# Kernel optimization log

Measured on AMD Instinct MI355X. Metric: run time of the kernel, lower is better.

## Reference

```python
import jax, jax.numpy as jnp
import numpy as np

B, Hh, Ww, C = 16, 56, 56, 256
NH, WS, SS = 8, 7, 3
HD = C // NH
N = WS * WS
SCALE = HD ** -0.5
EPS = 1e-5


def _rel_pos_index():
    coords = np.stack(np.meshgrid(np.arange(WS), np.arange(WS), indexing='ij'))  # (2, ws, ws)
    cf = coords.reshape(2, -1)
    rc = (cf[:, :, None] - cf[:, None, :]).transpose(1, 2, 0).astype(np.int64)  # (N, N, 2)
    rc[:, :, 0] += WS - 1
    rc[:, :, 1] += WS - 1
    rc[:, :, 0] *= 2 * WS - 1
    return jnp.asarray(rc.sum(-1))  # (N, N)

REL_IDX = _rel_pos_index()


def _shift_mask():
    # standard Swin SW-MSA mask for cyclic shift
    img = np.zeros((1, Hh, Ww, 1), dtype=np.float32)
    cnt = 0
    for hs in (slice(0, -WS), slice(-WS, -SS), slice(-SS, None)):
        for ws_ in (slice(0, -WS), slice(-WS, -SS), slice(-SS, None)):
            img[:, hs, ws_, :] = cnt
            cnt += 1
    mw = img.reshape(1, Hh // WS, WS, Ww // WS, WS, 1).transpose(0, 1, 3, 2, 4, 5).reshape(-1, N)
    am = mw[:, None, :] - mw[:, :, None]
    return jnp.asarray(np.where(am != 0, -100.0, 0.0).astype(np.float32))  # (nW, N, N)


def _ln(x, g, b):
    mu = x.mean(-1, keepdims=True)
    var = ((x - mu) ** 2).mean(-1, keepdims=True)
    return (x - mu) * jax.lax.rsqrt(var + EPS) * g + b


def setup_inputs() -> dict:
    key = jax.random.key(0)
    ks = jax.random.split(key, 8)
    return {
        'x': jax.random.normal(ks[0], (B, Hh * Ww, C), jnp.float32),
        'mask': _shift_mask(),
        'norm1_g': jnp.ones((C,), jnp.float32),
        'norm1_b': jnp.zeros((C,), jnp.float32),
        'qkv_w': jax.random.normal(ks[1], (3 * C, C), jnp.float32) * 0.02,
        'qkv_b': jnp.zeros((3 * C,), jnp.float32),
        'rel_bias': jax.random.normal(ks[2], ((2 * WS - 1) ** 2, NH), jnp.float32) * 0.02,
        'proj_w': jax.random.normal(ks[3], (C, C), jnp.float32) * 0.02,
        'proj_b': jnp.zeros((C,), jnp.float32),
        'norm2_g': jnp.ones((C,), jnp.float32),
        'norm2_b': jnp.zeros((C,), jnp.float32),
        'fc1_w': jax.random.normal(ks[4], (4 * C, C), jnp.float32) * 0.02,
        'fc1_b': jnp.zeros((4 * C,), jnp.float32),
        'fc2_w': jax.random.normal(ks[5], (C, 4 * C), jnp.float32) * 0.02,
        'fc2_b': jnp.zeros((C,), jnp.float32),
    }


def reference(x, mask, norm1_g, norm1_b, qkv_w, qkv_b, rel_bias, proj_w, proj_b,
              norm2_g, norm2_b, fc1_w, fc1_b, fc2_w, fc2_b):
    shortcut = x
    h = _ln(x, norm1_g, norm1_b).reshape(B, Hh, Ww, C)
    # cyclic shift
    h = jnp.roll(h, (-SS, -SS), axis=(1, 2))
    # window partition -> (B*nW, N, C)
    hw = h.reshape(B, Hh // WS, WS, Ww // WS, WS, C).transpose(0, 1, 3, 2, 4, 5).reshape(-1, N, C)
    # qkv projection
    qkv = (hw @ qkv_w.T + qkv_b).reshape(-1, N, 3, NH, HD).transpose(2, 0, 3, 1, 4)
    q, k, v = qkv[0] * SCALE, qkv[1], qkv[2]  # (Bw, NH, N, HD)
    attn = jnp.einsum('bhnd,bhmd->bhnm', q, k)  # (Bw, NH, N, N)
    rpb = rel_bias[REL_IDX.reshape(-1)].reshape(N, N, NH).transpose(2, 0, 1)
    attn = attn + rpb[None]
    nW = mask.shape[0]
    attn = attn.reshape(B, nW, NH, N, N) + mask[None, :, None]
    attn = jax.nn.softmax(attn.reshape(-1, NH, N, N), axis=-1)
    o = jnp.einsum('bhnm,bhmd->bhnd', attn, v).transpose(0, 2, 1, 3).reshape(-1, N, C)
    o = o @ proj_w.T + proj_b
    # window reverse
    o = o.reshape(B, Hh // WS, Ww // WS, WS, WS, C).transpose(0, 1, 3, 2, 4, 5).reshape(B, Hh, Ww, C)
    o = jnp.roll(o, (SS, SS), axis=(1, 2)).reshape(B, Hh * Ww, C)
    x = shortcut + o
    h2 = _ln(x, norm2_g, norm2_b)
    h2 = jax.nn.gelu(h2 @ fc1_w.T + fc1_b, approximate=False)
    return x + (h2 @ fc2_w.T + fc2_b)
```

## Files before the change

### kernel.cpp

```cpp
#include <hip/hip_runtime.h>
#include <cmath>

#define B_    16
#define HH    56
#define WWI   56
#define C_    256
#define NH_   8
#define WS_   7
#define SS_   3
#define HD_   32
#define NTOK  50176
#define NN    49
#define SCALE_ 0.17677669529663689f
#define EPS_  1e-5f

typedef __bf16  bf16x8  __attribute__((ext_vector_type(8)));
typedef float   f32x4   __attribute__((ext_vector_type(4)));
typedef unsigned short ushort8v __attribute__((ext_vector_type(8)));

__device__ __forceinline__ unsigned short f2bf(float f) {
    unsigned int u = __float_as_uint(f);
    unsigned int r = u + 0x7FFFu + ((u >> 16) & 1u);
    return (unsigned short)(r >> 16);
}
__device__ __forceinline__ float bf2f(unsigned short h) {
    return __uint_as_float(((unsigned int)h) << 16);
}
__device__ __forceinline__ float gelu_t(float x) {
    float t = 0.7978845608028654f * (x + 0.044715f * x * x * x);
    float e = __expf(2.0f * t);
    float th = 1.0f - 2.0f * __builtin_amdgcn_rcpf(e + 1.0f);
    return 0.5f * x * (1.0f + th);
}

__device__ __forceinline__ void gload_lds16(const unsigned short* g, unsigned short* l) {
    __builtin_amdgcn_global_load_lds(
        (const __attribute__((address_space(1))) unsigned int*)g,
        (__attribute__((address_space(3))) unsigned int*)l, 16, 0, 0);
}

__global__ __launch_bounds__(256) void convw_k(
    const float* __restrict__ qkvw, const float* __restrict__ projw,
    const float* __restrict__ fc1w, const float* __restrict__ fc2w,
    unsigned short* __restrict__ dst)
{
    int i = blockIdx.x * 256 + threadIdx.x;
    float v;
    if      (i < 196608) v = qkvw[i];
    else if (i < 262144) v = projw[i - 196608];
    else if (i < 524288) v = fc1w[i - 262144];
    else                 v = fc2w[i - 524288];
    dst[i] = f2bf(v);
}

__global__ __launch_bounds__(256) void cb_k(
    const float* __restrict__ mask, const float* __restrict__ relb,
    unsigned short* __restrict__ cb)
{
    int s = blockIdx.x;
    int wi = s >> 3, head = s & 7;
    for (int p = threadIdx.x; p < 2408; p += 256) {
        float v = 0.0f;
        if (p < 2401) {
            int i = p / NN, j = p - i * NN;
            int di = i / 7 - j / 7 + 6, dj = i % 7 - j % 7 + 6;
            v = relb[(di * 13 + dj) * NH_ + head] + mask[(size_t)wi * 2401 + p];
        }
        cb[(size_t)s * 2408 + p] = f2bf(v);
    }
}

__global__ __launch_bounds__(256) void ln_k(
    const float* __restrict__ x, const float* __restrict__ g,
    const float* __restrict__ bta, unsigned short* __restrict__ dst, int shifted)
{
    int wave = threadIdx.x >> 6, lane = threadIdx.x & 63;
    int tok = blockIdx.x * 4 + wave;
    const float4 v = *(const float4*)(x + (size_t)tok * C_ + lane * 4);
    float s = v.x + v.y + v.z + v.w;
    float q = v.x*v.x + v.y*v.y + v.z*v.z + v.w*v.w;
    for (int o = 32; o > 0; o >>= 1) { s += __shfl_xor(s, o, 64); q += __shfl_xor(q, o, 64); }
    float mu  = s * (1.0f / C_);
    float var = q * (1.0f / C_) - mu * mu;
    float rs  = rsqrtf(var + EPS_);
    float4 gg = *(const float4*)(g   + lane * 4);
    float4 bb = *(const float4*)(bta + lane * 4);
    float y0 = (v.x - mu) * rs * gg.x + bb.x;
    float y1 = (v.y - mu) * rs * gg.y + bb.y;
    float y2 = (v.z - mu) * rs * gg.z + bb.z;
    float y3 = (v.w - mu) * rs * gg.w + bb.w;
    size_t di;
    if (shifted) {
        int b = tok / 3136, p = tok % 3136;
        int ph = p / 56, pw = p % 56;
        int sh = ph - SS_; if (sh < 0) sh += HH;
        int sw = pw - SS_; if (sw < 0) sw += WWI;
        int bw = b * 64 + (sh / WS_) * 8 + (sw / WS_);
        int n  = (sh % WS_) * WS_ + (sw % WS_);
        di = ((size_t)bw * NN + n) * C_ + lane * 4;
    } else {
        di = (size_t)tok * C_ + lane * 4;
    }
    unsigned int lo = (unsigned int)f2bf(y0) | ((unsigned int)f2bf(y1) << 16);
    unsigned int hi = (unsigned int)f2bf(y2) | ((unsigned int)f2bf(y3) << 16);
    uint2 u; u.x = lo; u.y = hi;
    *(uint2*)(dst + di) = u;
}

template<int EPI, int NT>
__global__ __launch_bounds__(256) void gemm_k(
    const unsigned short* __restrict__ A, const unsigned short* __restrict__ Bt,
    int K, const float* __restrict__ bias,
    const float* __restrict__ resid, float* __restrict__ outF,
    unsigned short* __restrict__ outQ, unsigned short* __restrict__ outK,
    unsigned short* __restrict__ outV)
{
    __shared__ __align__(16) unsigned char smem[49152];
    const int tid = threadIdx.x;
    const int lin = blockIdx.x;
    const int xcd = lin & 7, t = lin >> 3;
    const int m0 = (xcd * 49 + t / NT) * 128;
    const int n0 = (t % NT) * 128;
    const int wave = tid >> 6, lane = tid & 63, quad = lane >> 4, l16 = lane & 15;
    const int wm = wave >> 1, wn = wave & 1;
    const int r0 = tid >> 2, c0 = (tid & 3) * 8;

    const size_t gA0 = (size_t)(m0 + r0) * K + c0;
    const size_t gA1 = (size_t)(m0 + r0 + 64) * K + c0;
    const size_t gB0 = (size_t)(n0 + r0) * K + c0;
    const size_t gB1 = (size_t)(n0 + r0 + 64) * K + c0;
    const int woff = wave * 512;

    f32x4 acc[4][4] = {};
    const int nk = K >> 5;
    #pragma unroll
    for (int p = 0; p < 2; ++p) {
        unsigned short* sA = (unsigned short*)(smem + p * 16384);
        unsigned short* sB = sA + 4096;
        const int kp = p << 5;
        gload_lds16(A + gA0 + kp, sA + woff);
        gload_lds16(A + gA1 + kp, sA + woff + 2048);
        gload_lds16(Bt + gB0 + kp, sB + woff);
        gload_lds16(Bt + gB1 + kp, sB + woff + 2048);
    }
    int bufc = 0;
    for (int kk = 0; kk < nk; ++kk) {
        if (kk + 2 < nk) {
            int bufn = bufc + 2; if (bufn >= 3) bufn -= 3;
            unsigned short* sA = (unsigned short*)(smem + bufn * 16384);
            unsigned short* sB = sA + 4096;
            const int k2 = (kk + 2) << 5;
            gload_lds16(A + gA0 + k2, sA + woff);
            gload_lds16(A + gA1 + k2, sA + woff + 2048);
            gload_lds16(Bt + gB0 + k2, sB + woff);
            gload_lds16(Bt + gB1 + k2, sB + woff + 2048);
            __asm volatile("s_waitcnt vmcnt(8)\n\ts_barrier" ::: "memory");
        } else if (kk + 1 < nk) {
            __asm volatile("s_waitcnt vmcnt(4)\n\ts_barrier" ::: "memory");
        } else {
            __asm volatile("s_waitcnt vmcnt(0)\n\ts_barrier" ::: "memory");
        }
        const unsigned short* sA = (const unsigned short*)(smem + bufc * 16384);
        const unsigned short* sB = sA + 4096;
        bf16x8 af[4], bfr[4];
        #pragma unroll
        for (int tt = 0; tt < 4; ++tt) {
            af[tt]  = __builtin_bit_cast(bf16x8, *(const ushort8v*)(sA + (wm * 64 + tt * 16 + l16) * 32 + quad * 8));
            bfr[tt] = __builtin_bit_cast(bf16x8, *(const ushort8v*)(sB + (wn * 64 + tt * 16 + l16) * 32 + quad * 8));
        }
        #pragma unroll
        for (int mt = 0; mt < 4; ++mt)
            #pragma unroll
            for (int nt = 0; nt < 4; ++nt)
                acc[mt][nt] = __builtin_amdgcn_mfma_f32_16x16x32_bf16(af[mt], bfr[nt], acc[mt][nt], 0, 0, 0);
        __asm volatile("s_barrier" ::: "memory");
        if (++bufc == 3) bufc = 0;
    }

    float b4[4];
    #pragma unroll
    for (int nt = 0; nt < 4; ++nt) b4[nt] = bias[n0 + wn * 64 + nt * 16 + l16];

    if (EPI == 0 || EPI == 2) {
        unsigned short (*swB)[136] = (unsigned short (*)[136])smem;
        const int seg = n0 >> 8;
        const float qs = (EPI == 0 && seg == 0) ? SCALE_ : 1.0f;
        #pragma unroll
        for (int mt = 0; mt < 4; ++mt)
            #pragma unroll
            for (int nt = 0; nt < 4; ++nt)
                #pragma unroll
                for (int r = 0; r < 4; ++r) {
                    float v = acc[mt][nt][r] + b4[nt];
                    if (EPI == 0) v *= qs; else v = gelu_t(v);
                    swB[wm * 64 + mt * 16 + quad * 4 + r][wn * 64 + nt * 16 + l16] = f2bf(v);
                }
        __syncthreads();
        if (EPI == 0) {
            unsigned short* dstp = seg == 0 ? outQ : (seg == 1 ? outK : outV);
            const int nbase = n0 & 255;
            for (int tt = tid; tt < 2048; tt += 256) {
                int row = tt >> 4, c8 = (tt & 15) * 8;
                int m = m0 + row, bw = m / NN, nw = m - bw * NN;
                int cc = nbase + c8;
                uint4 u = *(uint4*)&swB[row][c8];
                *(uint4*)&dstp[(((size_t)bw * NH_ + (cc >> 5)) * NN + nw) * HD_ + (cc & 31)] = u;
            }
        } else {
            for (int tt = tid; tt < 2048; tt += 256) {
                int row = tt >> 4, c8 = (tt & 15) * 8;
                uint4 u = *(uint4*)&swB[row][c8];
                *(uint4*)&outQ[(size_t)(m0 + row) * 1024 + n0 + c8] = u;
            }
        }
    } else {
        float (*swF)[132] = (float (*)[132])smem;
        #pragma unroll
        for (int p = 0; p < 2; ++p) {
            __syncthreads();
            if (wm == p) {
                #pragma unroll
                for (int mt = 0; mt < 4; ++mt)
                    #pragma unroll
                    for (int nt = 0; nt < 4; ++nt)
                        #pragma unroll
                        for (int r = 0; r < 4; ++r)
                            swF[mt * 16 + quad * 4 + r][wn * 64 + nt * 16 + l16] = acc[mt][nt][r] + b4[nt];
            }
            __syncthreads();
            for (int tt = tid; tt < 2048; tt += 256) {
                int rl = tt >> 5, c4 = (tt & 31) * 4;
                size_t adr;
                if (EPI == 1) {
                    int m = m0 + p * 64 + rl, bw = m / NN, nw = m - bw * NN;
                    int b = bw >> 6, wi = bw & 63;
                    int sh = (wi >> 3) * WS_ + nw / WS_;
                    int sw = (wi & 7) * WS_ + nw % WS_;
                    int ph = sh + SS_; if (ph >= HH)  ph -= HH;
                    int pw = sw + SS_; if (pw >= WWI) pw -= WWI;
                    adr = ((size_t)b * 3136 + ph * 56 + pw) * C_ + n0 + c4;
                } else {
                    adr = (size_t)(m0 + p * 64 + rl) * C_ + n0 + c4;
                }
                float4 u = *(float4*)&swF[rl][c4];
                const float4 rr = (EPI == 1) ? *(const float4*)&resid[adr]
                                             : *(const float4*)&outF[adr];
                u.x += rr.x; u.y += rr.y; u.z += rr.z; u.w += rr.w;
                *(float4*)&outF[adr] = u;
            }
        }
    }
}

__global__ __launch_bounds__(256) void attn_k(
    const unsigned short* __restrict__ qb, const unsigned short* __restrict__ kb,
    const unsigned short* __restrict__ vb, const unsigned short* __restrict__ cb,
    unsigned short* __restrict__ ob)
{
    __shared__ unsigned short qs[64][40];
    __shared__ unsigned short ks[64][40];
    __shared__ unsigned short vt[32][72];
    __shared__ unsigned short sp[64][72];
    __shared__ unsigned short cbs[2408];
    const int tid = threadIdx.x;
    const int bw = blockIdx.x >> 3, head = blockIdx.x & 7;
    const size_t base = (size_t)blockIdx.x * (NN * HD_);

    for (int t = tid; t < 588; t += 256) {
        int seg = t / 196, idx = t - seg * 196;
        int e = idx * 8;
        const unsigned short* src = (seg == 0 ? qb : seg == 1 ? kb : vb) + base + e;
        uint4 u = *(const uint4*)src;
        if (seg == 0)      *(uint4*)&qs[e >> 5][e & 31] = u;
        else if (seg == 1) *(uint4*)&ks[e >> 5][e & 31] = u;
        else {
            int n = e >> 5, hd = e & 31;
            const unsigned short* pu = (const unsigned short*)&u;
            #pragma unroll
            for (int uu = 0; uu < 8; ++uu) vt[hd + uu][n] = pu[uu];
        }
    }
    {
        const unsigned short* cbase = cb + (size_t)(((bw & 63) * 8 + head)) * 2408;
        for (int t = tid; t < 301; t += 256)
            *(uint4*)&cbs[t * 8] = *(const uint4*)(cbase + t * 8);
        for (int t = tid; t < 480; t += 256) vt[t / 15][NN + t % 15] = 0;
    }
    __syncthreads();

    const int wave = tid >> 6, lane = tid & 63, quad = lane >> 4, l16 = lane & 15;
    const f32x4 zz = {};

    bf16x8 afq = __builtin_bit_cast(bf16x8, *(const ushort8v*)&qs[wave * 16 + l16][quad * 8]);
    f32x4 s4[4];
    #pragma unroll
    for (int jt = 0; jt < 4; ++jt) {
        bf16x8 bk = __builtin_bit_cast(bf16x8, *(const ushort8v*)&ks[jt * 16 + l16][quad * 8]);
        s4[jt] = __builtin_amdgcn_mfma_f32_16x16x32_bf16(afq, bk, zz, 0, 0, 0);
    }

    #pragma unroll
    for (int r = 0; r < 4; ++r) {
        int i = wave * 16 + quad * 4 + r;
        float vals[4];
        #pragma unroll
        for (int jt = 0; jt < 4; ++jt) {
            int j = jt * 16 + l16;
            vals[jt] = (i < NN && j < NN) ? s4[jt][r] + bf2f(cbs[i * NN + j]) : -1e30f;
        }
        float mx = fmaxf(fmaxf(vals[0], vals[1]), fmaxf(vals[2], vals[3]));
        #pragma unroll
        for (int o = 1; o < 16; o <<= 1) mx = fmaxf(mx, __shfl_xor(mx, o, 64));
        float e[4], sum = 0.0f;
        #pragma unroll
        for (int jt = 0; jt < 4; ++jt) { e[jt] = __expf(vals[jt] - mx); sum += e[jt]; }
        #pragma unroll
        for (int o = 1; o < 16; o <<= 1) sum += __shfl_xor(sum, o, 64);
        float inv = 1.0f / sum;
        #pragma unroll
        for (int jt = 0; jt < 4; ++jt) sp[i][jt * 16 + l16] = f2bf(e[jt] * inv);
    }
    __syncthreads();

    bf16x8 ap[2];
    #pragma unroll
    for (int kt = 0; kt < 2; ++kt)
        ap[kt] = __builtin_bit_cast(bf16x8, *(const ushort8v*)&sp[wave * 16 + l16][kt * 32 + quad * 8]);
    f32x4 o4[2] = {};
    #pragma unroll
    for (int nt = 0; nt < 2; ++nt)
        #pragma unroll
        for (int kt = 0; kt < 2; ++kt) {
            bf16x8 bv = __builtin_bit_cast(bf16x8, *(const ushort8v*)&vt[nt * 16 + l16][kt * 32 + quad * 8]);
            o4[nt] = __builtin_amdgcn_mfma_f32_16x16x32_bf16(ap[kt], bv, o4[nt], 0, 0, 0);
        }
    #pragma unroll
    for (int nt = 0; nt < 2; ++nt)
        #pragma unroll
        for (int r = 0; r < 4; ++r) {
            int i = wave * 16 + quad * 4 + r;
            if (i < NN)
                ob[((size_t)bw * NN + i) * C_ + head * HD_ + nt * 16 + l16] = f2bf(o4[nt][r]);
        }
}

extern "C" void kernel_launch(void* const* d_in, const int* in_sizes, int n_in,
                              void* d_out, int out_size, void* d_ws, size_t ws_size,
                              hipStream_t stream)
{
    const float* x     = (const float*)d_in[0];
    const float* mask  = (const float*)d_in[1];
    const float* n1g   = (const float*)d_in[2];
    const float* n1b   = (const float*)d_in[3];
    const float* qkvw  = (const float*)d_in[4];
    const float* qkvb  = (const float*)d_in[5];
    const float* relb  = (const float*)d_in[6];
    const float* projw = (const float*)d_in[7];
    const float* projb = (const float*)d_in[8];
    const float* n2g   = (const float*)d_in[9];
    const float* n2b   = (const float*)d_in[10];
    const float* fc1w  = (const float*)d_in[11];
    const float* fc1b  = (const float*)d_in[12];
    const float* fc2w  = (const float*)d_in[13];
    const float* fc2b  = (const float*)d_in[14];
    float* out = (float*)d_out;

    unsigned short* wq = (unsigned short*)d_ws;
    unsigned short* wp = wq + 196608;
    unsigned short* w1 = wq + 262144;
    unsigned short* w2 = wq + 524288;
    unsigned short* hw = wq + 786432;
    unsigned short* qb = hw + 12845056;
    unsigned short* kb = qb + 12845056;
    unsigned short* vb = kb + 12845056;
    unsigned short* ob = vb + 12845056;
    unsigned short* h2 = ob + 12845056;
    unsigned short* a1 = h2 + 12845056;
    unsigned short* cbt = a1;

    convw_k<<<3072, 256, 0, stream>>>(qkvw, projw, fc1w, fc2w, wq);
    cb_k<<<512, 256, 0, stream>>>(mask, relb, cbt);
    ln_k<<<12544, 256, 0, stream>>>(x, n1g, n1b, hw, 1);
    gemm_k<0, 6><<<392 * 6, 256, 0, stream>>>(hw, wq, 256, qkvb, nullptr, nullptr, qb, kb, vb);
    attn_k<<<8192, 256, 0, stream>>>(qb, kb, vb, cbt, ob);
    gemm_k<1, 2><<<392 * 2, 256, 0, stream>>>(ob, wp, 256, projb, x, out, nullptr, nullptr, nullptr);
    ln_k<<<12544, 256, 0, stream>>>(out, n2g, n2b, h2, 0);
    gemm_k<2, 8><<<392 * 8, 256, 0, stream>>>(h2, w1, 256, fc1b, nullptr, nullptr, a1, nullptr, nullptr);
    gemm_k<3, 2><<<392 * 2, 256, 0, stream>>>(a1, w2, 1024, fc2b, nullptr, out, nullptr, nullptr, nullptr);
}
```

Baseline: 367.3 us.

## Rewrite GEMM to 256x256 tiles, 8 waves, BK=64, swizzled LDS

Replaces the 128x128, 4-wave, BK=32 triple-buffered GEMM with a 256x256 tile computed by 8 waves. It uses BK=64, double buffering, an XOR-swizzled LDS layout and s_setprio around the MFMA bursts. The block-to-XCD mapping is reworked to spread tiles contiguously per XCD. The goal is more data reuse per tile and fewer LDS bank conflicts. In exchange it needs 128KB of LDS, and the proj and fc2 GEMMs now launch only 196 workgroups, which may underfill the GPU.

Measured after the change: 420.0 us. +14.3%, slower.

```diff
diff --git a/kernel.cpp b/kernel.cpp
--- a/kernel.cpp
+++ b/kernel.cpp
@@ -37,6 +37,10 @@
     __builtin_amdgcn_global_load_lds(
         (const __attribute__((address_space(1))) unsigned int*)g,
         (__attribute__((address_space(3))) unsigned int*)l, 16, 0, 0);
+}
+
+__device__ __forceinline__ bf16x8 ld8(const unsigned char* p) {
+    return __builtin_bit_cast(bf16x8, *(const ushort8v*)p);
 }
 
 __global__ __launch_bounds__(256) void convw_k(
@@ -108,131 +112,150 @@
 }
 
 template<int EPI, int NT>
-__global__ __launch_bounds__(256) void gemm_k(
+__global__ __launch_bounds__(512, 2) void gemm_k(
     const unsigned short* __restrict__ A, const unsigned short* __restrict__ Bt,
     int K, const float* __restrict__ bias,
     const float* __restrict__ resid, float* __restrict__ outF,
     unsigned short* __restrict__ outQ, unsigned short* __restrict__ outK,
     unsigned short* __restrict__ outV)
 {
-    __shared__ __align__(16) unsigned char smem[49152];
-    const int tid = threadIdx.x;
-    const int lin = blockIdx.x;
-    const int xcd = lin & 7, t = lin >> 3;
-    const int m0 = (xcd * 49 + t / NT) * 128;
-    const int n0 = (t % NT) * 128;
-    const int wave = tid >> 6, lane = tid & 63, quad = lane >> 4, l16 = lane & 15;
-    const int wm = wave >> 1, wn = wave & 1;
-    const int r0 = tid >> 2, c0 = (tid & 3) * 8;
-
-    const size_t gA0 = (size_t)(m0 + r0) * K + c0;
-    const size_t gA1 = (size_t)(m0 + r0 + 64) * K + c0;
-    const size_t gB0 = (size_t)(n0 + r0) * K + c0;
-    const size_t gB1 = (size_t)(n0 + r0 + 64) * K + c0;
-    const int woff = wave * 512;
-
-    f32x4 acc[4][4] = {};
-    const int nk = K >> 5;
-    #pragma unroll
-    for (int p = 0; p < 2; ++p) {
-        unsigned short* sA = (unsigned short*)(smem + p * 16384);
-        unsigned short* sB = sA + 4096;
-        const int kp = p << 5;
-        gload_lds16(A + gA0 + kp, sA + woff);
-        gload_lds16(A + gA1 + kp, sA + woff + 2048);
-        gload_lds16(Bt + gB0 + kp, sB + woff);
-        gload_lds16(Bt + gB1 + kp, sB + woff + 2048);
-    }
-    int bufc = 0;
-    for (int kk = 0; kk < nk; ++kk) {
-        if (kk + 2 < nk) {
-            int bufn = bufc + 2; if (bufn >= 3) bufn -= 3;
-            unsigned short* sA = (unsigned short*)(smem + bufn * 16384);
-            unsigned short* sB = sA + 4096;
-            const int k2 = (kk + 2) << 5;
-            gload_lds16(A + gA0 + k2, sA + woff);
-            gload_lds16(A + gA1 + k2, sA + woff + 2048);
-            gload_lds16(Bt + gB0 + k2, sB + woff);
-            gload_lds16(Bt + gB1 + k2, sB + woff + 2048);
-            __asm volatile("s_waitcnt vmcnt(8)\n\ts_barrier" ::: "memory");
-        } else if (kk + 1 < nk) {
-            __asm volatile("s_waitcnt vmcnt(4)\n\ts_barrier" ::: "memory");
+    __shared__ __align__(16) unsigned char smem[131072];
+    const int tid  = threadIdx.x;
+    const int wave = tid >> 6, lane = tid & 63;
+    const int quad = lane >> 4, l16 = lane & 15;
+    const int nwg = 196 * NT;
+    const int qq = nwg >> 3, rr = nwg & 7;
+    const int xcd = blockIdx.x & 7, idx = blockIdx.x >> 3;
+    const int wg = (xcd < rr ? xcd * (qq + 1) : rr * (qq + 1) + (xcd - rr) * qq) + idx;
+    const int m0 = (wg / NT) * 256;
+    const int n0 = (wg % NT) * 256;
+    const int wm = wave >> 2, wn = wave & 3;
+
+    const int r8  = lane >> 3;
+    const int csl = (lane & 7) ^ r8;
+    const size_t aA = (size_t)(m0 + wave * 32 + r8) * K + csl * 8;
+    const size_t aB = (size_t)(n0 + wave * 32 + r8) * K + csl * 8;
+
+    f32x4 acc[8][4] = {};
+
+    #define STAGE(kt_, p_) { \
+        const unsigned short* sa_ = A  + aA + (size_t)(kt_) * 64; \
+        const unsigned short* sb_ = Bt + aB + (size_t)(kt_) * 64; \
+        unsigned char* da_ = smem + (p_) * 65536 + wave * 4096; \
+        unsigned char* db_ = da_ + 32768; \
+        _Pragma("unroll") \
+        for (int i_ = 0; i_ < 4; ++i_) { \
+            gload_lds16(sa_ + (size_t)i_ * 8 * K, (unsigned short*)(da_ + i_ * 1024)); \
+            gload_lds16(sb_ + (size_t)i_ * 8 * K, (unsigned short*)(db_ + i_ * 1024)); } }
+
+    STAGE(0, 0);
+    float b4[4];
+    #pragma unroll
+    for (int nt = 0; nt < 4; ++nt) b4[nt] = bias[n0 + wn * 64 + nt * 16 + l16];
+
+    const int nkt = K >> 6;
+    for (int kt = 0; kt < nkt; ++kt) {
+        const int p = kt & 1;
+        if (kt + 1 < nkt) {
+            STAGE(kt + 1, p ^ 1);
+            __asm volatile("s_waitcnt vmcnt(8)" ::: "memory");
         } else {
-            __asm volatile("s_waitcnt vmcnt(0)\n\ts_barrier" ::: "memory");
-        }
-        const unsigned short* sA = (const unsigned short*)(smem + bufc * 16384);
-        const unsigned short* sB = sA + 4096;
-        bf16x8 af[4], bfr[4];
-        #pragma unroll
-        for (int tt = 0; tt < 4; ++tt) {
-            af[tt]  = __builtin_bit_cast(bf16x8, *(const ushort8v*)(sA + (wm * 64 + tt * 16 + l16) * 32 + quad * 8));
-            bfr[tt] = __builtin_bit_cast(bf16x8, *(const ushort8v*)(sB + (wn * 64 + tt * 16 + l16) * 32 + quad * 8));
-        }
-        #pragma unroll
-        for (int mt = 0; mt < 4; ++mt)
+            __asm volatile("s_waitcnt vmcnt(0)" ::: "memory");
+        }
+        __asm volatile("s_barrier" ::: "memory");
+        const unsigned char* pa = smem + p * 65536;
+        const unsigned char* pb = pa + 32768;
+        bf16x8 bfr[4][2];
+        #pragma unroll
+        for (int nt = 0; nt < 4; ++nt)
             #pragma unroll
-            for (int nt = 0; nt < 4; ++nt)
-                acc[mt][nt] = __builtin_amdgcn_mfma_f32_16x16x32_bf16(af[mt], bfr[nt], acc[mt][nt], 0, 0, 0);
-        __asm volatile("s_barrier" ::: "memory");
-        if (++bufc == 3) bufc = 0;
-    }
-
-    float b4[4];
-    #pragma unroll
-    for (int nt = 0; nt < 4; ++nt) b4[nt] = bias[n0 + wn * 64 + nt * 16 + l16];
+            for (int kh = 0; kh < 2; ++kh) {
+                const int row = wn * 64 + nt * 16 + l16;
+                const int ch  = kh * 4 + quad;
+                bfr[nt][kh] = ld8(pb + row * 128 + ((ch ^ (row & 7)) << 4));
+            }
+        #pragma unroll
+        for (int q = 0; q < 4; ++q) {
+            bf16x8 af[2][2];
+            #pragma unroll
+            for (int dm = 0; dm < 2; ++dm)
+                #pragma unroll
+                for (int kh = 0; kh < 2; ++kh) {
+                    const int row = wm * 128 + (q * 2 + dm) * 16 + l16;
+                    const int ch  = kh * 4 + quad;
+                    af[dm][kh] = ld8(pa + row * 128 + ((ch ^ (row & 7)) << 4));
+                }
+            __builtin_amdgcn_s_setprio(1);
+            #pragma unroll
+            for (int dm = 0; dm < 2; ++dm)
+                #pragma unroll
+                for (int nt = 0; nt < 4; ++nt)
+                    #pragma unroll
+                    for (int kh = 0; kh < 2; ++kh)
+                        acc[q * 2 + dm][nt] = __builtin_amdgcn_mfma_f32_16x16x32_bf16(
+                            af[dm][kh], bfr[nt][kh], acc[q * 2 + dm][nt], 0, 0, 0);
+            __builtin_amdgcn_s_setprio(0);
+            __asm volatile("s_barrier" ::: "memory");
+        }
+    }
+    #undef STAGE
 
     if (EPI == 0 || EPI == 2) {
-        unsigned short (*swB)[136] = (unsigned short (*)[136])smem;
+        unsigned short (*swB)[264] = (unsigned short (*)[264])smem;
         const int seg = n0 >> 8;
         const float qs = (EPI == 0 && seg == 0) ? SCALE_ : 1.0f;
-        #pragma unroll
-        for (int mt = 0; mt < 4; ++mt)
-            #pragma unroll
-            for (int nt = 0; nt < 4; ++nt)
-                #pragma unroll
-                for (int r = 0; r < 4; ++r) {
-                    float v = acc[mt][nt][r] + b4[nt];
-                    if (EPI == 0) v *= qs; else v = gelu_t(v);
-                    swB[wm * 64 + mt * 16 + quad * 4 + r][wn * 64 + nt * 16 + l16] = f2bf(v);
-                }
-        __syncthreads();
-        if (EPI == 0) {
-            unsigned short* dstp = seg == 0 ? outQ : (seg == 1 ? outK : outV);
-            const int nbase = n0 & 255;
-            for (int tt = tid; tt < 2048; tt += 256) {
-                int row = tt >> 4, c8 = (tt & 15) * 8;
-                int m = m0 + row, bw = m / NN, nw = m - bw * NN;
-                int cc = nbase + c8;
-                uint4 u = *(uint4*)&swB[row][c8];
-                *(uint4*)&dstp[(((size_t)bw * NH_ + (cc >> 5)) * NN + nw) * HD_ + (cc & 31)] = u;
-            }
-        } else {
-            for (int tt = tid; tt < 2048; tt += 256) {
-                int row = tt >> 4, c8 = (tt & 15) * 8;
-                uint4 u = *(uint4*)&swB[row][c8];
-                *(uint4*)&outQ[(size_t)(m0 + row) * 1024 + n0 + c8] = u;
-            }
-        }
-    } else {
-        float (*swF)[132] = (float (*)[132])smem;
         #pragma unroll
         for (int p = 0; p < 2; ++p) {
             __syncthreads();
             if (wm == p) {
                 #pragma unroll
-                for (int mt = 0; mt < 4; ++mt)
+                for (int mt = 0; mt < 8; ++mt)
+                    #pragma unroll
+                    for (int nt = 0; nt < 4; ++nt)
+                        #pragma unroll
+                        for (int r = 0; r < 4; ++r) {
+                            float v = acc[mt][nt][r] + b4[nt];
+                            if (EPI == 0) v *= qs; else v = gelu_t(v);
+                            swB[mt * 16 + quad * 4 + r][wn * 64 + nt * 16 + l16] = f2bf(v);
+                        }
+            }
+            __syncthreads();
+            for (int tt = tid; tt < 4096; tt += 512) {
+                int row = tt >> 5, c8 = (tt & 31) * 8;
+                uint4 u = *(uint4*)&swB[row][c8];
+                int m = m0 + p * 128 + row;
+                if (EPI == 0) {
+                    int bw = m / NN, nw = m - bw * NN;
+                    unsigned short* dstp = seg == 0 ? outQ : (seg == 1 ? outK : outV);
+                    *(uint4*)&dstp[(((size_t)bw * NH_ + (c8 >> 5)) * NN + nw) * HD_ + (c8 & 31)] = u;
+                } else {
+                    *(uint4*)&outQ[(size_t)m * 1024 + n0 + c8] = u;
+                }
+            }
+        }
+    } else {
+        float (*swF)[260] = (float (*)[260])smem;
+        #pragma unroll
+        for (int p = 0; p < 4; ++p) {
+            __syncthreads();
+            if (wm == (p >> 1)) {
+                const int mtb = (p & 1) * 4;
+                #pragma unroll
+                for (int dm = 0; dm < 4; ++dm)
                     #pragma unroll
                     for (int nt = 0; nt < 4; ++nt)
                         #pragma unroll
                         for (int r = 0; r < 4; ++r)
-                            swF[mt * 16 + quad * 4 + r][wn * 64 + nt * 16 + l16] = acc[mt][nt][r] + b4[nt];
+                            swF[dm * 16 + quad * 4 + r][wn * 64 + nt * 16 + l16] =
+                                acc[mtb + dm][nt][r] + b4[nt];
             }
             __syncthreads();
-            for (int tt = tid; tt < 2048; tt += 256) {
-                int rl = tt >> 5, c4 = (tt & 31) * 4;
+            for (int tt = tid; tt < 4096; tt += 512) {
+                int rl = tt >> 6, c4 = (tt & 63) * 4;
+                int m = m0 + p * 64 + rl;
                 size_t adr;
                 if (EPI == 1) {
-                    int m = m0 + p * 64 + rl, bw = m / NN, nw = m - bw * NN;
+                    int bw = m / NN, nw = m - bw * NN;
                     int b = bw >> 6, wi = bw & 63;
                     int sh = (wi >> 3) * WS_ + nw / WS_;
                     int sw = (wi & 7) * WS_ + nw % WS_;
@@ -240,12 +263,12 @@
                     int pw = sw + SS_; if (pw >= WWI) pw -= WWI;
                     adr = ((size_t)b * 3136 + ph * 56 + pw) * C_ + n0 + c4;
                 } else {
-                    adr = (size_t)(m0 + p * 64 + rl) * C_ + n0 + c4;
+                    adr = (size_t)m * C_ + n0 + c4;
                 }
                 float4 u = *(float4*)&swF[rl][c4];
-                const float4 rr = (EPI == 1) ? *(const float4*)&resid[adr]
-                                             : *(const float4*)&outF[adr];
-                u.x += rr.x; u.y += rr.y; u.z += rr.z; u.w += rr.w;
+                const float4 rr2 = (EPI == 1) ? *(const float4*)&resid[adr]
+                                              : *(const float4*)&outF[adr];
+                u.x += rr2.x; u.y += rr2.y; u.z += rr2.z; u.w += rr2.w;
                 *(float4*)&outF[adr] = u;
             }
         }
@@ -381,10 +404,10 @@
     convw_k<<<3072, 256, 0, stream>>>(qkvw, projw, fc1w, fc2w, wq);
     cb_k<<<512, 256, 0, stream>>>(mask, relb, cbt);
     ln_k<<<12544, 256, 0, stream>>>(x, n1g, n1b, hw, 1);
-    gemm_k<0, 6><<<392 * 6, 256, 0, stream>>>(hw, wq, 256, qkvb, nullptr, nullptr, qb, kb, vb);
+    gemm_k<0, 3><<<588, 512, 0, stream>>>(hw, wq, 256, qkvb, nullptr, nullptr, qb, kb, vb);
     attn_k<<<8192, 256, 0, stream>>>(qb, kb, vb, cbt, ob);
-    gemm_k<1, 2><<<392 * 2, 256, 0, stream>>>(ob, wp, 256, projb, x, out, nullptr, nullptr, nullptr);
+    gemm_k<1, 1><<<196, 512, 0, stream>>>(ob, wp, 256, projb, x, out, nullptr, nullptr, nullptr);
     ln_k<<<12544, 256, 0, stream>>>(out, n2g, n2b, h2, 0);
-    gemm_k<2, 8><<<392 * 8, 256, 0, stream>>>(h2, w1, 256, fc1b, nullptr, nullptr, a1, nullptr, nullptr);
-    gemm_k<3, 2><<<392 * 2, 256, 0, stream>>>(a1, w2, 1024, fc2b, nullptr, out, nullptr, nullptr, nullptr);
-}
+    gemm_k<2, 4><<<784, 512, 0, stream>>>(h2, w1, 256, fc1b, nullptr, nullptr, a1, nullptr, nullptr);
+    gemm_k<3, 1><<<196, 512, 0, stream>>>(a1, w2, 1024, fc2b, nullptr, out, nullptr, nullptr, nullptr);
+}
```
